# Performance work log

Hardware: AMD Instinct MI355X
Metric: run time of the kernel (lower is better)

Reference implementation:

```python
import jax, jax.numpy as jnp
import numpy as np

N_LOC = 500000
N_CAT = 5000
N_EDGES = 2000000
LOC_DIM = 128
CAT_DIM = 128
INITRANGE = 0.1
NEG_SLOPE = 0.2


def setup_inputs() -> dict:
    key = jax.random.key(0)
    k1, k2, k3, k4 = jax.random.split(key, 4)
    loc_emb = jax.random.normal(k1, (N_LOC, LOC_DIM), dtype=jnp.float32)
    # loc_to_cat Linear params, init per init_weights(): uniform(-0.1, 0.1) weight, zero bias
    W = jax.random.uniform(k2, (CAT_DIM, LOC_DIM), dtype=jnp.float32,
                           minval=-INITRANGE, maxval=INITRANGE)
    b = jnp.zeros((CAT_DIM,), dtype=jnp.float32)
    edge_src = jax.random.randint(k3, (N_EDGES,), 0, N_LOC, dtype=jnp.int64)
    edge_dst = jax.random.randint(k4, (N_EDGES,), 0, N_CAT, dtype=jnp.int64)
    return {"loc_emb": loc_emb, "W": W, "b": b,
            "edge_src": edge_src, "edge_dst": edge_dst}


def reference(loc_emb, W, b, edge_src, edge_dst):
    # copy_u('f','m') + sum('m','in') across all canonical etypes, combined with 'sum':
    # gather source (loc) features along edges, segment-sum into cat nodes.
    msg = loc_emb[edge_src]                                   # [E, loc_dim]
    agg = jax.ops.segment_sum(msg, edge_dst, num_segments=N_CAT)  # [n_cat, loc_dim]
    # loc_to_cat linear + LeakyReLU(0.2)
    cat_emb = jax.nn.leaky_relu(agg @ W.T + b, negative_slope=NEG_SLOPE)
    return cat_emb
```

## Files before the change

### kernel.cpp

```cpp
#include <hip/hip_runtime.h>

#define N_LOC   500000
#define N_CAT   5000
#define N_EDGES 2000000
#define DIM     128
#define NEG_SLOPE 0.2f
#define PAD     5008
#define NB      256
#define EPB     7816
#define NC1     (N_CAT + 1)
#define SLIST   2048

__launch_bounds__(1024)
__global__ void build_kernel(const int* __restrict__ esrc, const int* __restrict__ edst,
                             const float* __restrict__ W, float* __restrict__ WT,
                             int* __restrict__ csr2, int* __restrict__ loffg) {
    int b = blockIdx.x, t = threadIdx.x;
    if (b == NB) {
        for (int i = t; i < DIM * DIM; i += 1024) {
            int j = i >> 7, k = i & 127;
            WT[k * DIM + j] = W[j * DIM + k];
        }
        return;
    }
    __shared__ int lh[N_CAT];
    __shared__ __align__(16) int sbuf[EPB];
    __shared__ int wsum[16], woff[16];

    for (int c2 = t; c2 < N_CAT; c2 += 1024) lh[c2] = 0;
    __syncthreads();

    const int s0 = b * EPB;
    const int len = min(s0 + EPB, N_EDGES) - s0;
    const int* dp = edst + s0;
    const int* sp = esrc + s0;

    #pragma unroll
    for (int j = 0; j < 2; ++j) {
        int off = j * 4096 + 4 * t;
        if (off < len) {
            int4 d = *(const int4*)(dp + off);
            atomicAdd(&lh[d.x], 1); atomicAdd(&lh[d.y], 1);
            atomicAdd(&lh[d.z], 1); atomicAdd(&lh[d.w], 1);
        }
    }
    __syncthreads();

    int lane = t & 63, w = t >> 6;
    int base = t * 5;
    int v0 = 0, v1 = 0, v2 = 0, v3 = 0, v4 = 0;
    if (base < N_CAT) { v0 = lh[base]; v1 = lh[base+1]; v2 = lh[base+2]; v3 = lh[base+3]; v4 = lh[base+4]; }
    int sum = v0 + v1 + v2 + v3 + v4;
    int incl = sum;
    #pragma unroll
    for (int o = 1; o < 64; o <<= 1) { int x = __shfl_up(incl, o, 64); if (lane >= o) incl += x; }
    if (lane == 63) wsum[w] = incl;
    __syncthreads();
    if (t < 16) {
        int sv = wsum[t]; int ev = sv;
        #pragma unroll
        for (int o = 1; o < 16; o <<= 1) { int x = __shfl_up(ev, o, 64); if (t >= o) ev += x; }
        woff[t] = ev - sv;
    }
    __syncthreads();
    if (base < N_CAT) {
        int run = woff[w] + (incl - sum);
        lh[base]     = run; run += v0;
        lh[base + 1] = run; run += v1;
        lh[base + 2] = run; run += v2;
        lh[base + 3] = run; run += v3;
        lh[base + 4] = run;
    }
    __syncthreads();

    for (int c2 = t; c2 < N_CAT; c2 += 1024) loffg[(size_t)b * NC1 + c2] = lh[c2];
    if (t == 0) loffg[(size_t)b * NC1 + N_CAT] = len;
    __syncthreads();

    #pragma unroll
    for (int j = 0; j < 2; ++j) {
        int off = j * 4096 + 4 * t;
        if (off < len) {
            int4 d = *(const int4*)(dp + off);
            int4 s = *(const int4*)(sp + off);
            int p0 = atomicAdd(&lh[d.x], 1); sbuf[p0] = s.x;
            int p1 = atomicAdd(&lh[d.y], 1); sbuf[p1] = s.y;
            int p2 = atomicAdd(&lh[d.z], 1); sbuf[p2] = s.z;
            int p3 = atomicAdd(&lh[d.w], 1); sbuf[p3] = s.w;
        }
    }
    __syncthreads();

    int* cout = csr2 + s0;
    for (int i = 4 * t; i < len; i += 4096)
        *(int4*)(cout + i) = *(const int4*)(sbuf + i);
}

__launch_bounds__(256)
__global__ void agg3_kernel(const float* __restrict__ loc, const int* __restrict__ csr2,
                            const int* __restrict__ loffg, const float* __restrict__ WT,
                            const float* __restrict__ bias, float* __restrict__ out) {
    __shared__ float4 sacc[256];
    __shared__ float  srow[DIM];
    __shared__ int    slist[SLIST];
    __shared__ int    wsum4[4], woff4[4], tot_s;
    int bid = blockIdx.x;
    int c = (bid & 7) * (N_CAT / 8) + (bid >> 3);
    int t = threadIdx.x;
    int lane = t & 63, w = t >> 6;

    int sOff = loffg[(size_t)t * NC1 + c];
    int cnt  = loffg[(size_t)t * NC1 + c + 1] - sOff;
    int incl = cnt;
    #pragma unroll
    for (int o = 1; o < 64; o <<= 1) { int x = __shfl_up(incl, o, 64); if (lane >= o) incl += x; }
    if (lane == 63) wsum4[w] = incl;
    __syncthreads();
    if (t == 0) {
        int r = 0;
        #pragma unroll
        for (int i = 0; i < 4; ++i) { woff4[i] = r; r += wsum4[i]; }
        tot_s = r;
    }
    __syncthreads();
    int sbase = woff4[w] + (incl - cnt);
    const int* seg = csr2 + (size_t)t * EPB + sOff;
    int lim = min(cnt, max(0, SLIST - sbase));
    for (int k = 0; k < lim; ++k) slist[sbase + k] = seg[k];
    __syncthreads();
    int total = min(tot_s, SLIST);

    int g = t >> 5;
    int l = t & 31;
    int per  = (total + 7) >> 3;
    int gbeg = g * per;
    int gend = min(gbeg + per, total);

    float4 a0 = make_float4(0.f, 0.f, 0.f, 0.f);
    float4 a1 = a0, a2 = a0, a3 = a0;
    int e = gbeg;
    for (; e + 8 <= gend; e += 8) {
        int s0 = slist[e + 0], s1 = slist[e + 1], s2 = slist[e + 2], s3 = slist[e + 3];
        int s4 = slist[e + 4], s5 = slist[e + 5], s6 = slist[e + 6], s7 = slist[e + 7];
        float4 v0 = ((const float4*)(loc + (size_t)s0 * DIM))[l];
        float4 v1 = ((const float4*)(loc + (size_t)s1 * DIM))[l];
        float4 v2 = ((const float4*)(loc + (size_t)s2 * DIM))[l];
        float4 v3 = ((const float4*)(loc + (size_t)s3 * DIM))[l];
        float4 v4 = ((const float4*)(loc + (size_t)s4 * DIM))[l];
        float4 v5 = ((const float4*)(loc + (size_t)s5 * DIM))[l];
        float4 v6 = ((const float4*)(loc + (size_t)s6 * DIM))[l];
        float4 v7 = ((const float4*)(loc + (size_t)s7 * DIM))[l];
        a0.x += v0.x; a0.y += v0.y; a0.z += v0.z; a0.w += v0.w;
        a1.x += v1.x; a1.y += v1.y; a1.z += v1.z; a1.w += v1.w;
        a2.x += v2.x; a2.y += v2.y; a2.z += v2.z; a2.w += v2.w;
        a3.x += v3.x; a3.y += v3.y; a3.z += v3.z; a3.w += v3.w;
        a0.x += v4.x; a0.y += v4.y; a0.z += v4.z; a0.w += v4.w;
        a1.x += v5.x; a1.y += v5.y; a1.z += v5.z; a1.w += v5.w;
        a2.x += v6.x; a2.y += v6.y; a2.z += v6.z; a2.w += v6.w;
        a3.x += v7.x; a3.y += v7.y; a3.z += v7.z; a3.w += v7.w;
    }
    for (; e + 4 <= gend; e += 4) {
        int s0 = slist[e + 0], s1 = slist[e + 1], s2 = slist[e + 2], s3 = slist[e + 3];
        float4 v0 = ((const float4*)(loc + (size_t)s0 * DIM))[l];
        float4 v1 = ((const float4*)(loc + (size_t)s1 * DIM))[l];
        float4 v2 = ((const float4*)(loc + (size_t)s2 * DIM))[l];
        float4 v3 = ((const float4*)(loc + (size_t)s3 * DIM))[l];
        a0.x += v0.x; a0.y += v0.y; a0.z += v0.z; a0.w += v0.w;
        a1.x += v1.x; a1.y += v1.y; a1.z += v1.z; a1.w += v1.w;
        a2.x += v2.x; a2.y += v2.y; a2.z += v2.z; a2.w += v2.w;
        a3.x += v3.x; a3.y += v3.y; a3.z += v3.z; a3.w += v3.w;
    }
    for (; e < gend; ++e) {
        int s = slist[e];
        float4 v = ((const float4*)(loc + (size_t)s * DIM))[l];
        a0.x += v.x; a0.y += v.y; a0.z += v.z; a0.w += v.w;
    }

    float4 acc = make_float4((a0.x + a1.x) + (a2.x + a3.x),
                             (a0.y + a1.y) + (a2.y + a3.y),
                             (a0.z + a1.z) + (a2.z + a3.z),
                             (a0.w + a1.w) + (a2.w + a3.w));
    sacc[t] = acc;
    __syncthreads();
    if (t < 128) {
        float4 a = sacc[t], b = sacc[t + 128];
        sacc[t] = make_float4(a.x + b.x, a.y + b.y, a.z + b.z, a.w + b.w);
    }
    __syncthreads();
    if (t < 64) {
        float4 a = sacc[t], b = sacc[t + 64];
        sacc[t] = make_float4(a.x + b.x, a.y + b.y, a.z + b.z, a.w + b.w);
    }
    __syncthreads();
    if (t < 32) {
        float4 a = sacc[t], b = sacc[t + 32];
        srow[4 * t + 0] = a.x + b.x;
        srow[4 * t + 1] = a.y + b.y;
        srow[4 * t + 2] = a.z + b.z;
        srow[4 * t + 3] = a.w + b.w;
    }
    __syncthreads();
    int j = t & 127;
    int h = t >> 7;
    float m0 = 0.f, m1 = 0.f, m2 = 0.f, m3 = 0.f;
    int k0 = h * 64;
    #pragma unroll 4
    for (int k = 0; k < 64; k += 4) {
        m0 += WT[(k0 + k + 0) * DIM + j] * srow[k0 + k + 0];
        m1 += WT[(k0 + k + 1) * DIM + j] * srow[k0 + k + 1];
        m2 += WT[(k0 + k + 2) * DIM + j] * srow[k0 + k + 2];
        m3 += WT[(k0 + k + 3) * DIM + j] * srow[k0 + k + 3];
    }
    float* sred = (float*)sacc;
    sred[t] = (m0 + m1) + (m2 + m3);
    __syncthreads();
    if (t < 128) {
        float v = sred[t] + sred[t + 128] + bias[t];
        v = v > 0.f ? v : NEG_SLOPE * v;
        out[(size_t)c * DIM + t] = v;
    }
}


__global__ void hist_rank_kernel(const int* __restrict__ dst, int* __restrict__ cnt,
                                 int* __restrict__ rank, int n) {
    int i = blockIdx.x * blockDim.x + threadIdx.x;
    if (i < n) rank[i] = atomicAdd(&cnt[dst[i]], 1);
}

__global__ void fill_rank_kernel(const int* __restrict__ src, const int* __restrict__ dst,
                                 const int* __restrict__ rank, const int* __restrict__ offsets,
                                 int* __restrict__ csr_src, int n) {
    int i = blockIdx.x * blockDim.x + threadIdx.x;
    if (i < n) csr_src[offsets[dst[i]] + rank[i]] = src[i];
}

__global__ void transpose_kernel(const float* __restrict__ W, float* __restrict__ WT) {
    int j = blockIdx.x;
    int k = threadIdx.x;
    WT[k * DIM + j] = W[j * DIM + k];
}

__global__ void zero_kernel(float* p, int n) {
    int i = blockIdx.x * blockDim.x + threadIdx.x;
    if (i < n) p[i] = 0.f;
}

__launch_bounds__(1024)
__global__ void scan_kernel(const int* __restrict__ cnt, int* __restrict__ offsets) {
    __shared__ int wsum[16];
    __shared__ int woff[16];
    __shared__ int total_s, running_s;
    int t = threadIdx.x;
    int lane = t & 63, w = t >> 6;
    if (t == 0) { running_s = 0; offsets[0] = 0; }
    __syncthreads();
    for (int base = 0; base < N_CAT; base += 1024) {
        int i = base + t;
        int v = (i < N_CAT) ? cnt[i] : 0;
        int incl = v;
        #pragma unroll
        for (int off = 1; off < 64; off <<= 1) {
            int x = __shfl_up(incl, off, 64);
            if (lane >= off) incl += x;
        }
        if (lane == 63) wsum[w] = incl;
        __syncthreads();
        if (w == 0 && lane < 16) {
            int s = wsum[lane];
            int e = s;
            #pragma unroll
            for (int off = 1; off < 16; off <<= 1) {
                int x = __shfl_up(e, off, 64);
                if (lane >= off) e += x;
            }
            woff[lane] = e - s;
            if (lane == 15) total_s = e;
        }
        __syncthreads();
        int run = running_s;
        if (i < N_CAT) offsets[i + 1] = run + woff[w] + incl;
        __syncthreads();
        if (t == 0) running_s = run + total_s;
        __syncthreads();
    }
}

__launch_bounds__(256)
__global__ void agg_fused_kernel(const float* __restrict__ loc, const int* __restrict__ csr_src,
                                 const int* __restrict__ offsets, const float* __restrict__ WT,
                                 const float* __restrict__ bias, float* __restrict__ out) {
    __shared__ float4 sacc[256];
    __shared__ float  srow[DIM];
    int c = blockIdx.x;
    int t = threadIdx.x;
    int g = t >> 5;
    int l = t & 31;
    int beg = offsets[c];
    int end = offsets[c + 1];
    int cnt = end - beg;
    int per = (cnt + 7) >> 3;
    int gbeg = beg + g * per;
    int gend = min(gbeg + per, end);

    float4 a0 = make_float4(0.f, 0.f, 0.f, 0.f);
    float4 a1 = a0, a2 = a0, a3 = a0;
    int e = gbeg;
    for (; e + 4 <= gend; e += 4) {
        int s0 = csr_src[e + 0], s1 = csr_src[e + 1], s2 = csr_src[e + 2], s3 = csr_src[e + 3];
        float4 v0 = ((const float4*)(loc + (size_t)s0 * DIM))[l];
        float4 v1 = ((const float4*)(loc + (size_t)s1 * DIM))[l];
        float4 v2 = ((const float4*)(loc + (size_t)s2 * DIM))[l];
        float4 v3 = ((const float4*)(loc + (size_t)s3 * DIM))[l];
        a0.x += v0.x; a0.y += v0.y; a0.z += v0.z; a0.w += v0.w;
        a1.x += v1.x; a1.y += v1.y; a1.z += v1.z; a1.w += v1.w;
        a2.x += v2.x; a2.y += v2.y; a2.z += v2.z; a2.w += v2.w;
        a3.x += v3.x; a3.y += v3.y; a3.z += v3.z; a3.w += v3.w;
    }
    for (; e < gend; ++e) {
        int s = csr_src[e];
        float4 v = ((const float4*)(loc + (size_t)s * DIM))[l];
        a0.x += v.x; a0.y += v.y; a0.z += v.z; a0.w += v.w;
    }
    float4 acc = make_float4((a0.x + a1.x) + (a2.x + a3.x),
                             (a0.y + a1.y) + (a2.y + a3.y),
                             (a0.z + a1.z) + (a2.z + a3.z),
                             (a0.w + a1.w) + (a2.w + a3.w));
    sacc[t] = acc;
    __syncthreads();
    if (t < 128) {
        float4 a = sacc[t], b = sacc[t + 128];
        sacc[t] = make_float4(a.x + b.x, a.y + b.y, a.z + b.z, a.w + b.w);
    }
    __syncthreads();
    if (t < 64) {
        float4 a = sacc[t], b = sacc[t + 64];
        sacc[t] = make_float4(a.x + b.x, a.y + b.y, a.z + b.z, a.w + b.w);
    }
    __syncthreads();
    if (t < 32) {
        float4 a = sacc[t], b = sacc[t + 32];
        srow[4 * t + 0] = a.x + b.x;
        srow[4 * t + 1] = a.y + b.y;
        srow[4 * t + 2] = a.z + b.z;
        srow[4 * t + 3] = a.w + b.w;
    }
    __syncthreads();
    int j = t & 127;
    int h = t >> 7;
    float m0 = 0.f, m1 = 0.f, m2 = 0.f, m3 = 0.f;
    int k0 = h * 64;
    #pragma unroll 4
    for (int k = 0; k < 64; k += 4) {
        m0 += WT[(k0 + k + 0) * DIM + j] * srow[k0 + k + 0];
        m1 += WT[(k0 + k + 1) * DIM + j] * srow[k0 + k + 1];
        m2 += WT[(k0 + k + 2) * DIM + j] * srow[k0 + k + 2];
        m3 += WT[(k0 + k + 3) * DIM + j] * srow[k0 + k + 3];
    }
    float* sred = (float*)sacc;
    sred[t] = (m0 + m1) + (m2 + m3);
    __syncthreads();
    if (t < 128) {
        float v = sred[t] + sred[t + 128] + bias[t];
        v = v > 0.f ? v : NEG_SLOPE * v;
        out[(size_t)c * DIM + t] = v;
    }
}

__launch_bounds__(128)
__global__ void scatter_atomic_kernel(const float* __restrict__ loc, const int* __restrict__ src,
                                      const int* __restrict__ dst, float* __restrict__ agg) {
    int e = blockIdx.x;
    int d = threadIdx.x;
    atomicAdd(&agg[(size_t)dst[e] * DIM + d], loc[(size_t)src[e] * DIM + d]);
}

#define CATS_PER_BLOCK 8
__launch_bounds__(256)
__global__ void gemm_lrelu_kernel(const float* __restrict__ agg, const float* __restrict__ W,
                                  const float* __restrict__ b, float* __restrict__ out) {
    __shared__ float sW[DIM * 129];
    __shared__ float sA[CATS_PER_BLOCK * DIM];
    int t = threadIdx.x;
    int cbase = blockIdx.x * CATS_PER_BLOCK;
    for (int i = t; i < DIM * DIM; i += 256) {
        int j = i >> 7, k = i & 127;
        sW[j * 129 + k] = W[i];
    }
    for (int i = t; i < CATS_PER_BLOCK * DIM; i += 256)
        sA[i] = agg[(size_t)cbase * DIM + i];
    __syncthreads();
    int j = t & 127;
    int cc = t >> 7;
    float acc0 = 0.f, acc1 = 0.f, acc2 = 0.f, acc3 = 0.f;
    for (int k = 0; k < DIM; ++k) {
        float w = sW[j * 129 + k];
        acc0 += w * sA[(cc + 0) * DIM + k];
        acc1 += w * sA[(cc + 2) * DIM + k];
        acc2 += w * sA[(cc + 4) * DIM + k];
        acc3 += w * sA[(cc + 6) * DIM + k];
    }
    float bj = b[j];
    float r0 = acc0 + bj, r1 = acc1 + bj, r2 = acc2 + bj, r3 = acc3 + bj;
    r0 = r0 > 0.f ? r0 : NEG_SLOPE * r0;
    r1 = r1 > 0.f ? r1 : NEG_SLOPE * r1;
    r2 = r2 > 0.f ? r2 : NEG_SLOPE * r2;
    r3 = r3 > 0.f ? r3 : NEG_SLOPE * r3;
    out[(size_t)(cbase + cc + 0) * DIM + j] = r0;
    out[(size_t)(cbase + cc + 2) * DIM + j] = r1;
    out[(size_t)(cbase + cc + 4) * DIM + j] = r2;
    out[(size_t)(cbase + cc + 6) * DIM + j] = r3;
}

extern "C" void kernel_launch(void* const* d_in, const int* in_sizes, int n_in,
                              void* d_out, int out_size, void* d_ws, size_t ws_size,
                              hipStream_t stream) {
    const float* loc  = (const float*)d_in[0];
    const float* W    = (const float*)d_in[1];
    const float* bias = (const float*)d_in[2];
    const int*   esrc = (const int*)d_in[3];
    const int*   edst = (const int*)d_in[4];
    float* out = (float*)d_out;

    size_t need_new  = ((size_t)N_EDGES + (size_t)NB * NC1 + DIM * DIM) * sizeof(int);
    size_t need_rank = ((size_t)2 * N_EDGES + 2 * PAD + DIM * DIM) * sizeof(int);

    if (ws_size >= need_new) {
        int*   csr2  = (int*)d_ws;
        int*   loffg = csr2 + N_EDGES;
        float* WT    = (float*)(loffg + (size_t)NB * NC1);

        build_kernel<<<NB + 1, 1024, 0, stream>>>(esrc, edst, W, WT, csr2, loffg);
        agg3_kernel<<<N_CAT, 256, 0, stream>>>(loc, csr2, loffg, WT, bias, out);
    } else if (ws_size >= need_rank) {
        int* counts  = (int*)d_ws;
        int* offsets = counts + PAD;
        float* WT    = (float*)(offsets + PAD);
        int* rank    = (int*)(WT + DIM * DIM);
        int* csr_src = rank + N_EDGES;

        hipMemsetAsync(counts, 0, (size_t)PAD * sizeof(int), stream);
        transpose_kernel<<<DIM, DIM, 0, stream>>>(W, WT);
        const int eblocks = (N_EDGES + 255) / 256;
        hist_rank_kernel<<<eblocks, 256, 0, stream>>>(edst, counts, rank, N_EDGES);
        scan_kernel<<<1, 1024, 0, stream>>>(counts, offsets);
        fill_rank_kernel<<<eblocks, 256, 0, stream>>>(esrc, edst, rank, offsets, csr_src, N_EDGES);
        agg_fused_kernel<<<N_CAT, 256, 0, stream>>>(loc, csr_src, offsets, WT, bias, out);
    } else {
        int n = N_CAT * DIM;
        zero_kernel<<<(n + 255) / 256, 256, 0, stream>>>(out, n);
        scatter_atomic_kernel<<<N_EDGES, DIM, 0, stream>>>(loc, esrc, edst, out);
        gemm_lrelu_kernel<<<N_CAT / CATS_PER_BLOCK, 256, 0, stream>>>(out, W, bias, out);
    }
}
```

Baseline: 457.1 us.

## Bucket per-category source lists by row-index quarter before gathering

The aggregation kernel now splits each category's source indices into four buckets by which quarter of the location table they fall in, using a packed two-counter prefix scan. It then gathers the buckets one after another so that, at any moment, blocks across the GPU tend to read from the same region of loc_emb. The aim is better L2/MALL locality for the random 128-float row gathers. The cost is an extra pass over each segment for counting and more branchy index placement.

Measured after the change: 458.3 us. About the same (+0.3%).

```diff
diff --git a/kernel.cpp b/kernel.cpp
--- a/kernel.cpp
+++ b/kernel.cpp
@@ -10,6 +10,7 @@
 #define EPB     7816
 #define NC1     (N_CAT + 1)
 #define SLIST   2048
+#define QTR     125000
 
 __launch_bounds__(1024)
 __global__ void build_kernel(const int* __restrict__ esrc, const int* __restrict__ edst,
@@ -97,13 +98,14 @@
 }
 
 __launch_bounds__(256)
-__global__ void agg3_kernel(const float* __restrict__ loc, const int* __restrict__ csr2,
+__global__ void agg4_kernel(const float* __restrict__ loc, const int* __restrict__ csr2,
                             const int* __restrict__ loffg, const float* __restrict__ WT,
                             const float* __restrict__ bias, float* __restrict__ out) {
     __shared__ float4 sacc[256];
     __shared__ float  srow[DIM];
     __shared__ int    slist[SLIST];
-    __shared__ int    wsum4[4], woff4[4], tot_s;
+    __shared__ int    wA[4], wB[4];
+    __shared__ int    Qb[5];
     int bid = blockIdx.x;
     int c = (bid & 7) * (N_CAT / 8) + (bid >> 3);
     int t = threadIdx.x;
@@ -111,69 +113,126 @@
 
     int sOff = loffg[(size_t)t * NC1 + c];
     int cnt  = loffg[(size_t)t * NC1 + c + 1] - sOff;
-    int incl = cnt;
-    #pragma unroll
-    for (int o = 1; o < 64; o <<= 1) { int x = __shfl_up(incl, o, 64); if (lane >= o) incl += x; }
-    if (lane == 63) wsum4[w] = incl;
-    __syncthreads();
+    const int* seg = csr2 + (size_t)t * EPB + sOff;
+
+    int vals[8];
+    #pragma unroll
+    for (int k = 0; k < 8; ++k) vals[k] = (k < cnt) ? seg[k] : 0;
+
+    int c0 = 0, c1 = 0, c2 = 0, c3 = 0;
+    #pragma unroll
+    for (int k = 0; k < 8; ++k) {
+        if (k < cnt) {
+            int s = vals[k];
+            if (s >= 2 * QTR) { if (s >= 3 * QTR) ++c3; else ++c2; }
+            else              { if (s >= QTR)     ++c1; else ++c0; }
+        }
+    }
+    for (int k = 8; k < cnt; ++k) {
+        int s = seg[k];
+        if (s >= 2 * QTR) { if (s >= 3 * QTR) ++c3; else ++c2; }
+        else              { if (s >= QTR)     ++c1; else ++c0; }
+    }
+    int A = c0 | (c1 << 16);
+    int B = c2 | (c3 << 16);
+    int iA = A, iB = B;
+    #pragma unroll
+    for (int o = 1; o < 64; o <<= 1) {
+        int x = __shfl_up(iA, o, 64);
+        int y = __shfl_up(iB, o, 64);
+        if (lane >= o) { iA += x; iB += y; }
+    }
+    if (lane == 63) { wA[w] = iA; wB[w] = iB; }
+    __syncthreads();
+    int baseA = 0, baseB = 0;
+    #pragma unroll
+    for (int i = 0; i < 4; ++i) if (i < w) { baseA += wA[i]; baseB += wB[i]; }
+    int totA = wA[0] + wA[1] + wA[2] + wA[3];
+    int totB = wB[0] + wB[1] + wB[2] + wB[3];
+    int eA = baseA + iA - A;
+    int eB = baseB + iB - B;
+    int T0 = totA & 0xffff, T1 = totA >> 16, T2 = totB & 0xffff, T3 = totB >> 16;
     if (t == 0) {
-        int r = 0;
-        #pragma unroll
-        for (int i = 0; i < 4; ++i) { woff4[i] = r; r += wsum4[i]; }
-        tot_s = r;
-    }
-    __syncthreads();
-    int sbase = woff4[w] + (incl - cnt);
-    const int* seg = csr2 + (size_t)t * EPB + sOff;
-    int lim = min(cnt, max(0, SLIST - sbase));
-    for (int k = 0; k < lim; ++k) slist[sbase + k] = seg[k];
-    __syncthreads();
-    int total = min(tot_s, SLIST);
+        Qb[0] = 0; Qb[1] = T0; Qb[2] = T0 + T1; Qb[3] = T0 + T1 + T2; Qb[4] = T0 + T1 + T2 + T3;
+    }
+    int cur0 = (eA & 0xffff);
+    int cur1 = T0 + (eA >> 16);
+    int cur2 = T0 + T1 + (eB & 0xffff);
+    int cur3 = T0 + T1 + T2 + (eB >> 16);
+    #pragma unroll
+    for (int k = 0; k < 8; ++k) {
+        if (k < cnt) {
+            int s = vals[k];
+            if (s >= 2 * QTR) {
+                if (s >= 3 * QTR) { if (cur3 < SLIST) slist[cur3] = s; ++cur3; }
+                else              { if (cur2 < SLIST) slist[cur2] = s; ++cur2; }
+            } else {
+                if (s >= QTR)     { if (cur1 < SLIST) slist[cur1] = s; ++cur1; }
+                else              { if (cur0 < SLIST) slist[cur0] = s; ++cur0; }
+            }
+        }
+    }
+    for (int k = 8; k < cnt; ++k) {
+        int s = seg[k];
+        if (s >= 2 * QTR) {
+            if (s >= 3 * QTR) { if (cur3 < SLIST) slist[cur3] = s; ++cur3; }
+            else              { if (cur2 < SLIST) slist[cur2] = s; ++cur2; }
+        } else {
+            if (s >= QTR)     { if (cur1 < SLIST) slist[cur1] = s; ++cur1; }
+            else              { if (cur0 < SLIST) slist[cur0] = s; ++cur0; }
+        }
+    }
+    __syncthreads();
 
     int g = t >> 5;
     int l = t & 31;
-    int per  = (total + 7) >> 3;
-    int gbeg = g * per;
-    int gend = min(gbeg + per, total);
-
     float4 a0 = make_float4(0.f, 0.f, 0.f, 0.f);
     float4 a1 = a0, a2 = a0, a3 = a0;
-    int e = gbeg;
-    for (; e + 8 <= gend; e += 8) {
-        int s0 = slist[e + 0], s1 = slist[e + 1], s2 = slist[e + 2], s3 = slist[e + 3];
-        int s4 = slist[e + 4], s5 = slist[e + 5], s6 = slist[e + 6], s7 = slist[e + 7];
-        float4 v0 = ((const float4*)(loc + (size_t)s0 * DIM))[l];
-        float4 v1 = ((const float4*)(loc + (size_t)s1 * DIM))[l];
-        float4 v2 = ((const float4*)(loc + (size_t)s2 * DIM))[l];
-        float4 v3 = ((const float4*)(loc + (size_t)s3 * DIM))[l];
-        float4 v4 = ((const float4*)(loc + (size_t)s4 * DIM))[l];
-        float4 v5 = ((const float4*)(loc + (size_t)s5 * DIM))[l];
-        float4 v6 = ((const float4*)(loc + (size_t)s6 * DIM))[l];
-        float4 v7 = ((const float4*)(loc + (size_t)s7 * DIM))[l];
-        a0.x += v0.x; a0.y += v0.y; a0.z += v0.z; a0.w += v0.w;
-        a1.x += v1.x; a1.y += v1.y; a1.z += v1.z; a1.w += v1.w;
-        a2.x += v2.x; a2.y += v2.y; a2.z += v2.z; a2.w += v2.w;
-        a3.x += v3.x; a3.y += v3.y; a3.z += v3.z; a3.w += v3.w;
-        a0.x += v4.x; a0.y += v4.y; a0.z += v4.z; a0.w += v4.w;
-        a1.x += v5.x; a1.y += v5.y; a1.z += v5.z; a1.w += v5.w;
-        a2.x += v6.x; a2.y += v6.y; a2.z += v6.z; a2.w += v6.w;
-        a3.x += v7.x; a3.y += v7.y; a3.z += v7.z; a3.w += v7.w;
-    }
-    for (; e + 4 <= gend; e += 4) {
-        int s0 = slist[e + 0], s1 = slist[e + 1], s2 = slist[e + 2], s3 = slist[e + 3];
-        float4 v0 = ((const float4*)(loc + (size_t)s0 * DIM))[l];
-        float4 v1 = ((const float4*)(loc + (size_t)s1 * DIM))[l];
-        float4 v2 = ((const float4*)(loc + (size_t)s2 * DIM))[l];
-        float4 v3 = ((const float4*)(loc + (size_t)s3 * DIM))[l];
-        a0.x += v0.x; a0.y += v0.y; a0.z += v0.z; a0.w += v0.w;
-        a1.x += v1.x; a1.y += v1.y; a1.z += v1.z; a1.w += v1.w;
-        a2.x += v2.x; a2.y += v2.y; a2.z += v2.z; a2.w += v2.w;
-        a3.x += v3.x; a3.y += v3.y; a3.z += v3.z; a3.w += v3.w;
-    }
-    for (; e < gend; ++e) {
-        int s = slist[e];
-        float4 v = ((const float4*)(loc + (size_t)s * DIM))[l];
-        a0.x += v.x; a0.y += v.y; a0.z += v.z; a0.w += v.w;
+
+    #pragma unroll 1
+    for (int q = 0; q < 4; ++q) {
+        int qs = min(Qb[q], SLIST);
+        int qe = min(Qb[q + 1], SLIST);
+        int qcnt = qe - qs;
+        int per  = (qcnt + 7) >> 3;
+        int e    = qs + g * per;
+        int ge   = min(e + per, qe);
+        for (; e + 8 <= ge; e += 8) {
+            int s0 = slist[e + 0], s1 = slist[e + 1], s2 = slist[e + 2], s3 = slist[e + 3];
+            int s4 = slist[e + 4], s5 = slist[e + 5], s6 = slist[e + 6], s7 = slist[e + 7];
+            float4 v0 = ((const float4*)(loc + (size_t)s0 * DIM))[l];
+            float4 v1 = ((const float4*)(loc + (size_t)s1 * DIM))[l];
+            float4 v2 = ((const float4*)(loc + (size_t)s2 * DIM))[l];
+            float4 v3 = ((const float4*)(loc + (size_t)s3 * DIM))[l];
+            float4 v4 = ((const float4*)(loc + (size_t)s4 * DIM))[l];
+            float4 v5 = ((const float4*)(loc + (size_t)s5 * DIM))[l];
+            float4 v6 = ((const float4*)(loc + (size_t)s6 * DIM))[l];
+            float4 v7 = ((const float4*)(loc + (size_t)s7 * DIM))[l];
+            a0.x += v0.x; a0.y += v0.y; a0.z += v0.z; a0.w += v0.w;
+            a1.x += v1.x; a1.y += v1.y; a1.z += v1.z; a1.w += v1.w;
+            a2.x += v2.x; a2.y += v2.y; a2.z += v2.z; a2.w += v2.w;
+            a3.x += v3.x; a3.y += v3.y; a3.z += v3.z; a3.w += v3.w;
+            a0.x += v4.x; a0.y += v4.y; a0.z += v4.z; a0.w += v4.w;
+            a1.x += v5.x; a1.y += v5.y; a1.z += v5.z; a1.w += v5.w;
+            a2.x += v6.x; a2.y += v6.y; a2.z += v6.z; a2.w += v6.w;
+            a3.x += v7.x; a3.y += v7.y; a3.z += v7.z; a3.w += v7.w;
+        }
+        for (; e + 4 <= ge; e += 4) {
+            int s0 = slist[e + 0], s1 = slist[e + 1], s2 = slist[e + 2], s3 = slist[e + 3];
+            float4 v0 = ((const float4*)(loc + (size_t)s0 * DIM))[l];
+            float4 v1 = ((const float4*)(loc + (size_t)s1 * DIM))[l];
+            float4 v2 = ((const float4*)(loc + (size_t)s2 * DIM))[l];
+            float4 v3 = ((const float4*)(loc + (size_t)s3 * DIM))[l];
+            a0.x += v0.x; a0.y += v0.y; a0.z += v0.z; a0.w += v0.w;
+            a1.x += v1.x; a1.y += v1.y; a1.z += v1.z; a1.w += v1.w;
+            a2.x += v2.x; a2.y += v2.y; a2.z += v2.z; a2.w += v2.w;
+            a3.x += v3.x; a3.y += v3.y; a3.z += v3.z; a3.w += v3.w;
+        }
+        for (; e < ge; ++e) {
+            int s = slist[e];
+            float4 v = ((const float4*)(loc + (size_t)s * DIM))[l];
+            a0.x += v.x; a0.y += v.y; a0.z += v.z; a0.w += v.w;
+        }
     }
 
     float4 acc = make_float4((a0.x + a1.x) + (a2.x + a3.x),
@@ -431,7 +490,7 @@
         float* WT    = (float*)(loffg + (size_t)NB * NC1);
 
         build_kernel<<<NB + 1, 1024, 0, stream>>>(esrc, edst, W, WT, csr2, loffg);
-        agg3_kernel<<<N_CAT, 256, 0, stream>>>(loc, csr2, loffg, WT, bias, out);
+        agg4_kernel<<<N_CAT, 256, 0, stream>>>(loc, csr2, loffg, WT, bias, out);
     } else if (ws_size >= need_rank) {
         int* counts  = (int*)d_ws;
         int* offsets = counts + PAD;
```

## Split aggregation into two passes by source-row range for cache locality

Applied to the files above, without the earlier changes.

The aggregation kernel now runs twice, each pass only gathering edges whose source row falls in one half of the location table (0..250k, 250k..500k). The first pass writes partial sums to a workspace buffer, and the second adds them before the linear layer and LeakyReLU. The intent is that each pass's working set of roughly 128 MB fits better in the last-level cache, so random row gathers hit cache more often. In exchange, each edge segment is scanned twice per pass for filtering, there is an extra kernel launch, and partial sums make a round trip through global memory.

After: 478.0 us. 4.6% more time.

```diff
diff --git a/kernel.cpp b/kernel.cpp
--- a/kernel.cpp
+++ b/kernel.cpp
@@ -10,6 +10,7 @@
 #define EPB     7816
 #define NC1     (N_CAT + 1)
 #define SLIST   2048
+#define HALF    250000
 
 __launch_bounds__(1024)
 __global__ void build_kernel(const int* __restrict__ esrc, const int* __restrict__ edst,
@@ -97,9 +98,10 @@
 }
 
 __launch_bounds__(256)
-__global__ void agg3_kernel(const float* __restrict__ loc, const int* __restrict__ csr2,
+__global__ void agg5_kernel(const float* __restrict__ loc, const int* __restrict__ csr2,
                             const int* __restrict__ loffg, const float* __restrict__ WT,
-                            const float* __restrict__ bias, float* __restrict__ out) {
+                            const float* __restrict__ bias, float* __restrict__ pagg,
+                            float* __restrict__ out, int lo, int hi, int final) {
     __shared__ float4 sacc[256];
     __shared__ float  srow[DIM];
     __shared__ int    slist[SLIST];
@@ -111,7 +113,14 @@
 
     int sOff = loffg[(size_t)t * NC1 + c];
     int cnt  = loffg[(size_t)t * NC1 + c + 1] - sOff;
-    int incl = cnt;
+    const int* seg = csr2 + (size_t)t * EPB + sOff;
+
+    int m = 0;
+    for (int k = 0; k < cnt; ++k) {
+        int s = seg[k];
+        m += (s >= lo && s < hi) ? 1 : 0;
+    }
+    int incl = m;
     #pragma unroll
     for (int o = 1; o < 64; o <<= 1) { int x = __shfl_up(incl, o, 64); if (lane >= o) incl += x; }
     if (lane == 63) wsum4[w] = incl;
@@ -123,10 +132,11 @@
         tot_s = r;
     }
     __syncthreads();
-    int sbase = woff4[w] + (incl - cnt);
-    const int* seg = csr2 + (size_t)t * EPB + sOff;
-    int lim = min(cnt, max(0, SLIST - sbase));
-    for (int k = 0; k < lim; ++k) slist[sbase + k] = seg[k];
+    int pos = woff4[w] + (incl - m);
+    for (int k = 0; k < cnt; ++k) {
+        int s = seg[k];
+        if (s >= lo && s < hi) { if (pos < SLIST) slist[pos] = s; ++pos; }
+    }
     __syncthreads();
     int total = min(tot_s, SLIST);
 
@@ -200,6 +210,14 @@
         srow[4 * t + 3] = a.w + b.w;
     }
     __syncthreads();
+
+    if (!final) {
+        if (t < 128) pagg[(size_t)c * DIM + t] = srow[t];
+        return;
+    }
+    if (t < 128) srow[t] += pagg[(size_t)c * DIM + t];
+    __syncthreads();
+
     int j = t & 127;
     int h = t >> 7;
     float m0 = 0.f, m1 = 0.f, m2 = 0.f, m3 = 0.f;
@@ -422,16 +440,18 @@
     const int*   edst = (const int*)d_in[4];
     float* out = (float*)d_out;
 
-    size_t need_new  = ((size_t)N_EDGES + (size_t)NB * NC1 + DIM * DIM) * sizeof(int);
+    size_t need_new  = ((size_t)N_EDGES + (size_t)NB * NC1 + DIM * DIM + (size_t)N_CAT * DIM) * sizeof(int);
     size_t need_rank = ((size_t)2 * N_EDGES + 2 * PAD + DIM * DIM) * sizeof(int);
 
     if (ws_size >= need_new) {
         int*   csr2  = (int*)d_ws;
         int*   loffg = csr2 + N_EDGES;
         float* WT    = (float*)(loffg + (size_t)NB * NC1);
+        float* pagg  = WT + DIM * DIM;
 
         build_kernel<<<NB + 1, 1024, 0, stream>>>(esrc, edst, W, WT, csr2, loffg);
-        agg3_kernel<<<N_CAT, 256, 0, stream>>>(loc, csr2, loffg, WT, bias, out);
+        agg5_kernel<<<N_CAT, 256, 0, stream>>>(loc, csr2, loffg, WT, bias, pagg, out, 0, HALF, 0);
+        agg5_kernel<<<N_CAT, 256, 0, stream>>>(loc, csr2, loffg, WT, bias, pagg, out, HALF, N_LOC, 1);
     } else if (ws_size >= need_rank) {
         int* counts  = (int*)d_ws;
         int* offsets = counts + PAD;
```
